# Kernel optimization log

Hardware: AMD Instinct MI355X
Metric: run time of the kernel (lower is better)

Reference implementation:

```python
import jax, jax.numpy as jnp
import numpy as np

N_NODES = 100000
N_EDGES = 1600000
HIDDEN = 64


def setup_inputs() -> dict:
    key = jax.random.key(0)
    ks = jax.random.split(key, 10)
    s = 0.1
    x = jax.random.normal(ks[0], (N_NODES, 1), dtype=jnp.float32)
    edge_index = jax.random.randint(ks[1], (2, N_EDGES), 0, N_NODES, dtype=jnp.int32)
    edge_weight = jnp.ones((N_EDGES,), dtype=jnp.float32)
    f32 = jnp.float32
    return {
        "x": x,
        "edge_weight": edge_weight,
        "Wz": jax.random.normal(ks[2], (1, HIDDEN), f32) * s,
        "bz": jnp.zeros((HIDDEN,), f32),
        "Lz": jax.random.normal(ks[3], (2 * HIDDEN, HIDDEN), f32) * s,
        "lbz": jnp.zeros((HIDDEN,), f32),
        "Wr": jax.random.normal(ks[4], (1, HIDDEN), f32) * s,
        "br": jnp.zeros((HIDDEN,), f32),
        "Lr": jax.random.normal(ks[5], (2 * HIDDEN, HIDDEN), f32) * s,
        "lbr": jnp.zeros((HIDDEN,), f32),
        "Wh": jax.random.normal(ks[6], (1, HIDDEN), f32) * s,
        "bh": jnp.zeros((HIDDEN,), f32),
        "Lh": jax.random.normal(ks[7], (2 * HIDDEN, HIDDEN), f32) * s,
        "lbh": jnp.zeros((HIDDEN,), f32),
        "Wout": jax.random.normal(ks[8], (HIDDEN, 1), f32) * s,
        "bout": jnp.zeros((1,), f32),
        "edge_index": edge_index,
    }


def reference(x, edge_weight, Wz, bz, Lz, lbz, Wr, br, Lr, lbr,
              Wh, bh, Lh, lbh, Wout, bout, edge_index):
    N = x.shape[0]
    hidden = Wz.shape[1]
    src, dst = edge_index[0], edge_index[1]
    # GCN normalization with added self-loops (PyG gcn_norm)
    loop = jnp.arange(N, dtype=src.dtype)
    src2 = jnp.concatenate([src, loop])
    dst2 = jnp.concatenate([dst, loop])
    ew2 = jnp.concatenate([edge_weight, jnp.ones((N,), x.dtype)])
    deg = jax.ops.segment_sum(ew2, dst2, num_segments=N)  # [N]
    dinv = jnp.where(deg > 0, jax.lax.rsqrt(deg), 0.0)
    norm = dinv[src2] * ew2 * dinv[dst2]  # [E+N]

    def gcn(W, b):
        xw = x @ W  # [N, H]
        agg = jax.ops.segment_sum(xw[src2] * norm[:, None], dst2, num_segments=N)
        return agg + b

    # TGCN cell with H0 = 0 (no hidden state passed)
    H = jnp.zeros((N, hidden), x.dtype)
    Z = jax.nn.sigmoid(jnp.concatenate([gcn(Wz, bz), H], axis=1) @ Lz + lbz)
    R = jax.nn.sigmoid(jnp.concatenate([gcn(Wr, br), H], axis=1) @ Lr + lbr)
    Ht = jnp.tanh(jnp.concatenate([gcn(Wh, bh), H * R], axis=1) @ Lh + lbh)
    Hn = Z * H + (1.0 - Z) * Ht
    h = jax.nn.relu(Hn)
    return h @ Wout + bout
```

## Files before the change

kernel.cpp:

```cpp
#include <hip/hip_runtime.h>
#include <math.h>

#define HIDDEN 64
#define RANGE 16384
#define RSHIFT 14
#define NRANGES 7
#define NP 256
#define CAP 1536
#define G 32
#define SUB (NP / G)
#define PACK_SHIFT 17

__global__ __launch_bounds__(512)
void k_part(const int* __restrict__ dst, const int* __restrict__ src,
            const float* __restrict__ ew, uint2* __restrict__ comp,
            int* __restrict__ counts, int E) {
    __shared__ int cur[8];
    if (threadIdx.x < NRANGES) cur[threadIdx.x] = 0;
    __syncthreads();

    const int b = blockIdx.x;
    long long e0 = (((long long)E * b) / NP) & ~3LL;
    long long e1 = (b == NP - 1) ? (long long)E
                                 : ((((long long)E * (b + 1)) / NP) & ~3LL);
    const int nvec = (int)((e1 - e0) >> 2);
    const int4*   dst4 = (const int4*)(dst + e0);
    const int4*   src4 = (const int4*)(src + e0);
    const float4* ew4  = (const float4*)(ew + e0);

    for (int i = threadIdx.x; i < nvec; i += blockDim.x) {
        int4   d = dst4[i];
        int4   s = src4[i];
        float4 t = ew4[i];
        int   dd[4] = {d.x, d.y, d.z, d.w};
        int   ss[4] = {s.x, s.y, s.z, s.w};
        float tt[4] = {t.x, t.y, t.z, t.w};
        #pragma unroll
        for (int j = 0; j < 4; ++j) {
            unsigned u = (unsigned)dd[j];
            int r = (int)(u >> RSHIFT);
            unsigned l = u & (RANGE - 1);
            int pos = atomicAdd(&cur[r], 1);
            if (pos < CAP)
                comp[((size_t)(r * NP + b)) * CAP + pos] =
                    make_uint2((l << PACK_SHIFT) | (unsigned)ss[j],
                               __float_as_uint(tt[j]));
        }
    }
    for (long long e = e0 + ((long long)nvec << 2) + threadIdx.x; e < e1;
         e += blockDim.x) {
        unsigned u = (unsigned)dst[e];
        int r = (int)(u >> RSHIFT);
        unsigned l = u & (RANGE - 1);
        int pos = atomicAdd(&cur[r], 1);
        if (pos < CAP)
            comp[((size_t)(r * NP + b)) * CAP + pos] =
                make_uint2((l << PACK_SHIFT) | (unsigned)src[e],
                           __float_as_uint(ew[e]));
    }
    __syncthreads();
    if (threadIdx.x < NRANGES)
        counts[threadIdx.x * NP + b] = min(cur[threadIdx.x], CAP);
}

__global__ __launch_bounds__(1024)
void k_deg(const uint2* __restrict__ comp, const int* __restrict__ counts,
           float* __restrict__ partials, int nranges) {
    __shared__ float bins[RANGE];
    float4* b4 = (float4*)bins;
    for (int i = threadIdx.x; i < RANGE / 4; i += blockDim.x)
        b4[i] = make_float4(0.f, 0.f, 0.f, 0.f);
    __syncthreads();

    const int r = blockIdx.x % nranges;
    const int c = blockIdx.x / nranges;
    #pragma unroll
    for (int sub = 0; sub < SUB; ++sub) {
        const int b = c * SUB + sub;
        const uint2* sl = comp + ((size_t)(r * NP + b)) * CAP;
        const int n = counts[r * NP + b];
        for (int i = threadIdx.x; i < n; i += blockDim.x) {
            uint2 e = sl[i];
            atomicAdd(&bins[e.x >> PACK_SHIFT], __uint_as_float(e.y));
        }
    }
    __syncthreads();
    float4* outp = (float4*)(partials + ((size_t)c * nranges + r) * RANGE);
    for (int i = threadIdx.x; i < RANGE / 4; i += blockDim.x) outp[i] = b4[i];
}

__global__ void k_node(const float* __restrict__ x, const float* __restrict__ partials,
                       float* __restrict__ dinv, float* __restrict__ w,
                       int N, int nranges,
                       const float* __restrict__ Wz, const float* __restrict__ bz,
                       const float* __restrict__ Lz, const float* __restrict__ lbz,
                       const float* __restrict__ Wh, const float* __restrict__ bh,
                       const float* __restrict__ Lh, const float* __restrict__ lbh,
                       float* __restrict__ coeff) {
    int i = blockIdx.x * blockDim.x + threadIdx.x;
    if (i < N) {
        int r = i >> RSHIFT, local = i & (RANGE - 1);
        const float* p = partials + (size_t)r * RANGE + local;
        float d = 1.0f;
        #pragma unroll
        for (int c = 0; c < G; ++c) d += p[(size_t)c * nranges * RANGE];
        float di = rsqrtf(d);
        dinv[i] = di;
        w[i] = di * x[i];
    }
    if (blockIdx.x == 0 && threadIdx.x < HIDDEN) {
        int j = threadIdx.x;
        float vz = 0.f, cz = 0.f, vh = 0.f, ch = 0.f;
        for (int k = 0; k < HIDDEN; ++k) {
            float lz = Lz[k * HIDDEN + j];
            float lh = Lh[k * HIDDEN + j];
            vz += Wz[k] * lz;
            cz += bz[k] * lz;
            vh += Wh[k] * lh;
            ch += bh[k] * lh;
        }
        coeff[j]       = vz;
        coeff[64 + j]  = cz + lbz[j];
        coeff[128 + j] = vh;
        coeff[192 + j] = ch + lbh[j];
    }
}

__global__ __launch_bounds__(1024)
void k_agg(const uint2* __restrict__ comp, const int* __restrict__ counts,
           const float* __restrict__ w, float* __restrict__ partials, int nranges) {
    __shared__ float bins[RANGE];
    float4* b4 = (float4*)bins;
    for (int i = threadIdx.x; i < RANGE / 4; i += blockDim.x)
        b4[i] = make_float4(0.f, 0.f, 0.f, 0.f);
    __syncthreads();

    const int r = blockIdx.x % nranges;
    const int c = blockIdx.x / nranges;
    #pragma unroll
    for (int sub = 0; sub < SUB; ++sub) {
        const int b = c * SUB + sub;
        const uint2* sl = comp + ((size_t)(r * NP + b)) * CAP;
        const int n = counts[r * NP + b];
        for (int i = threadIdx.x; i < n; i += blockDim.x) {
            uint2 e = sl[i];
            float v = w[e.x & ((1u << PACK_SHIFT) - 1u)] * __uint_as_float(e.y);
            atomicAdd(&bins[e.x >> PACK_SHIFT], v);
        }
    }
    __syncthreads();
    float4* outp = (float4*)(partials + ((size_t)c * nranges + r) * RANGE);
    for (int i = threadIdx.x; i < RANGE / 4; i += blockDim.x) outp[i] = b4[i];
}

__global__ void k_out(const float* __restrict__ partials, const float* __restrict__ dinv,
                      const float* __restrict__ w, const float* __restrict__ coeff,
                      const float* __restrict__ Wout, const float* __restrict__ bout,
                      float* __restrict__ out, int N, int nranges) {
    __shared__ float c[5 * HIDDEN];
    __shared__ float b0;
    if (threadIdx.x < 4 * HIDDEN) c[threadIdx.x] = coeff[threadIdx.x];
    if (threadIdx.x < HIDDEN) c[4 * HIDDEN + threadIdx.x] = Wout[threadIdx.x];
    if (threadIdx.x == 0) b0 = bout[0];
    __syncthreads();
    int i = blockIdx.x * blockDim.x + threadIdx.x;
    if (i < N) {
        int r = i >> RSHIFT, local = i & (RANGE - 1);
        const float* p = partials + (size_t)r * RANGE + local;
        float g = w[i];
        #pragma unroll
        for (int k = 0; k < G; ++k) g += p[(size_t)k * nranges * RANGE];
        float si = dinv[i] * g;
        float acc = b0;
        #pragma unroll
        for (int j = 0; j < HIDDEN; ++j) {
            float zp = fminf(fmaxf(si * c[j] + c[64 + j], -30.f), 30.f);
            float hp = fminf(fmaxf(si * c[128 + j] + c[192 + j], -15.f), 15.f);
            float a  = __expf(2.0f * hp);
            float t  = (a - 1.0f) / (a + 1.0f);
            float zn = 1.0f / (1.0f + __expf(zp));
            float hn = zn * t;
            hn = hn > 0.0f ? hn : 0.0f;
            acc = fmaf(hn, c[256 + j], acc);
        }
        out[i] = acc;
    }
}

extern "C" void kernel_launch(void* const* d_in, const int* in_sizes, int n_in,
                              void* d_out, int out_size, void* d_ws, size_t ws_size,
                              hipStream_t stream) {
    const float* x    = (const float*)d_in[0];
    const float* ew   = (const float*)d_in[1];
    const float* Wz   = (const float*)d_in[2];
    const float* bz   = (const float*)d_in[3];
    const float* Lz   = (const float*)d_in[4];
    const float* lbz  = (const float*)d_in[5];
    const float* Wh   = (const float*)d_in[10];
    const float* bh   = (const float*)d_in[11];
    const float* Lh   = (const float*)d_in[12];
    const float* lbh  = (const float*)d_in[13];
    const float* Wout = (const float*)d_in[14];
    const float* bout = (const float*)d_in[15];
    const int*   eidx = (const int*)d_in[16];

    const int N = in_sizes[0];
    const int E = in_sizes[1];
    const int* src = eidx;
    const int* dst = eidx + E;

    const int nranges = (N + RANGE - 1) / RANGE;

    float* partials = (float*)d_ws;
    uint2* comp     = (uint2*)(partials + (size_t)G * nranges * RANGE);
    float* dinv     = (float*)(comp + (size_t)NRANGES * NP * CAP);
    float* w        = dinv + N;
    float* coeff    = w + N;
    int*   counts   = (int*)(coeff + 4 * HIDDEN);

    const int TB = 256;
    const int grid_bin = nranges * G;

    k_part<<<NP, 512, 0, stream>>>(dst, src, ew, comp, counts, E);
    k_deg<<<grid_bin, 1024, 0, stream>>>(comp, counts, partials, nranges);
    k_node<<<(N + TB - 1) / TB, TB, 0, stream>>>(x, partials, dinv, w, N, nranges,
                                                 Wz, bz, Lz, lbz, Wh, bh, Lh, lbh, coeff);
    k_agg<<<grid_bin, 1024, 0, stream>>>(comp, counts, w, partials, nranges);
    k_out<<<(N + TB - 1) / TB, TB, 0, stream>>>(partials, dinv, w, coeff, Wout, bout,
                                                (float*)d_out, N, nranges);
}
```

Measured before the change: 155.3 us.

## Use fine-grained dst ranges so degree and aggregation fuse with node and output stages

Partitions edges into many small 512-node destination ranges instead of 7 large ones. Each block now owns one range, so degree accumulation writes dinv and w directly, and aggregation computes the final output in place. This removes the partials buffer, the reduction across 32 partial copies, and two kernel launches. The coefficient precompute moves into the partition kernel. The risks are a dynamic per-bucket capacity that could drop edges on skewed inputs, and a smaller grid (~196 blocks) that may underfill the GPU.

```diff
diff --git a/kernel.cpp b/kernel.cpp
--- a/kernel.cpp
+++ b/kernel.cpp
@@ -2,21 +2,24 @@
 #include <math.h>
 
 #define HIDDEN 64
-#define RANGE 16384
-#define RSHIFT 14
-#define NRANGES 7
+#define RANGE 512
+#define RSHIFT 9
 #define NP 256
-#define CAP 1536
-#define G 32
-#define SUB (NP / G)
+#define NRMAX 256
 #define PACK_SHIFT 17
+
 
 __global__ __launch_bounds__(512)
 void k_part(const int* __restrict__ dst, const int* __restrict__ src,
             const float* __restrict__ ew, uint2* __restrict__ comp,
-            int* __restrict__ counts, int E) {
-    __shared__ int cur[8];
-    if (threadIdx.x < NRANGES) cur[threadIdx.x] = 0;
+            int* __restrict__ counts,
+            const float* __restrict__ Wz, const float* __restrict__ bz,
+            const float* __restrict__ Lz, const float* __restrict__ lbz,
+            const float* __restrict__ Wh, const float* __restrict__ bh,
+            const float* __restrict__ Lh, const float* __restrict__ lbh,
+            float* __restrict__ coeff, int E, int nr, int cap) {
+    __shared__ int cur[NRMAX];
+    for (int i = threadIdx.x; i < nr; i += blockDim.x) cur[i] = 0;
     __syncthreads();
 
     const int b = blockIdx.x;
@@ -41,8 +44,8 @@
             int r = (int)(u >> RSHIFT);
             unsigned l = u & (RANGE - 1);
             int pos = atomicAdd(&cur[r], 1);
-            if (pos < CAP)
-                comp[((size_t)(r * NP + b)) * CAP + pos] =
+            if (pos < cap)
+                comp[((size_t)(r * NP + b)) * cap + pos] =
                     make_uint2((l << PACK_SHIFT) | (unsigned)ss[j],
                                __float_as_uint(tt[j]));
         }
@@ -53,62 +56,16 @@
         int r = (int)(u >> RSHIFT);
         unsigned l = u & (RANGE - 1);
         int pos = atomicAdd(&cur[r], 1);
-        if (pos < CAP)
-            comp[((size_t)(r * NP + b)) * CAP + pos] =
+        if (pos < cap)
+            comp[((size_t)(r * NP + b)) * cap + pos] =
                 make_uint2((l << PACK_SHIFT) | (unsigned)src[e],
                            __float_as_uint(ew[e]));
     }
     __syncthreads();
-    if (threadIdx.x < NRANGES)
-        counts[threadIdx.x * NP + b] = min(cur[threadIdx.x], CAP);
-}
-
-__global__ __launch_bounds__(1024)
-void k_deg(const uint2* __restrict__ comp, const int* __restrict__ counts,
-           float* __restrict__ partials, int nranges) {
-    __shared__ float bins[RANGE];
-    float4* b4 = (float4*)bins;
-    for (int i = threadIdx.x; i < RANGE / 4; i += blockDim.x)
-        b4[i] = make_float4(0.f, 0.f, 0.f, 0.f);
-    __syncthreads();
-
-    const int r = blockIdx.x % nranges;
-    const int c = blockIdx.x / nranges;
-    #pragma unroll
-    for (int sub = 0; sub < SUB; ++sub) {
-        const int b = c * SUB + sub;
-        const uint2* sl = comp + ((size_t)(r * NP + b)) * CAP;
-        const int n = counts[r * NP + b];
-        for (int i = threadIdx.x; i < n; i += blockDim.x) {
-            uint2 e = sl[i];
-            atomicAdd(&bins[e.x >> PACK_SHIFT], __uint_as_float(e.y));
-        }
-    }
-    __syncthreads();
-    float4* outp = (float4*)(partials + ((size_t)c * nranges + r) * RANGE);
-    for (int i = threadIdx.x; i < RANGE / 4; i += blockDim.x) outp[i] = b4[i];
-}
-
-__global__ void k_node(const float* __restrict__ x, const float* __restrict__ partials,
-                       float* __restrict__ dinv, float* __restrict__ w,
-                       int N, int nranges,
-                       const float* __restrict__ Wz, const float* __restrict__ bz,
-                       const float* __restrict__ Lz, const float* __restrict__ lbz,
-                       const float* __restrict__ Wh, const float* __restrict__ bh,
-                       const float* __restrict__ Lh, const float* __restrict__ lbh,
-                       float* __restrict__ coeff) {
-    int i = blockIdx.x * blockDim.x + threadIdx.x;
-    if (i < N) {
-        int r = i >> RSHIFT, local = i & (RANGE - 1);
-        const float* p = partials + (size_t)r * RANGE + local;
-        float d = 1.0f;
-        #pragma unroll
-        for (int c = 0; c < G; ++c) d += p[(size_t)c * nranges * RANGE];
-        float di = rsqrtf(d);
-        dinv[i] = di;
-        w[i] = di * x[i];
-    }
-    if (blockIdx.x == 0 && threadIdx.x < HIDDEN) {
+    for (int rr = threadIdx.x; rr < nr; rr += blockDim.x)
+        counts[rr * NP + b] = min(cur[rr], cap);
+
+    if (b == 0 && threadIdx.x < HIDDEN) {
         int j = threadIdx.x;
         float vz = 0.f, cz = 0.f, vh = 0.f, ch = 0.f;
         for (int k = 0; k < HIDDEN; ++k) {
@@ -126,64 +83,88 @@
     }
 }
 
-__global__ __launch_bounds__(1024)
-void k_agg(const uint2* __restrict__ comp, const int* __restrict__ counts,
-           const float* __restrict__ w, float* __restrict__ partials, int nranges) {
+__global__ __launch_bounds__(512)
+void k_degw(const uint2* __restrict__ comp, const int* __restrict__ counts,
+            const float* __restrict__ x, float* __restrict__ dinv,
+            float* __restrict__ w, int N, int cap) {
     __shared__ float bins[RANGE];
-    float4* b4 = (float4*)bins;
-    for (int i = threadIdx.x; i < RANGE / 4; i += blockDim.x)
-        b4[i] = make_float4(0.f, 0.f, 0.f, 0.f);
-    __syncthreads();
-
-    const int r = blockIdx.x % nranges;
-    const int c = blockIdx.x / nranges;
-    #pragma unroll
-    for (int sub = 0; sub < SUB; ++sub) {
-        const int b = c * SUB + sub;
-        const uint2* sl = comp + ((size_t)(r * NP + b)) * CAP;
-        const int n = counts[r * NP + b];
-        for (int i = threadIdx.x; i < n; i += blockDim.x) {
+    __shared__ int cnt[NP];
+    const int r = blockIdx.x;
+    for (int i = threadIdx.x; i < RANGE; i += blockDim.x) bins[i] = 1.0f;
+    for (int i = threadIdx.x; i < NP; i += blockDim.x) cnt[i] = counts[r * NP + i];
+    __syncthreads();
+
+    const int wave = threadIdx.x >> 6, lane = threadIdx.x & 63;
+    const int nw = blockDim.x >> 6;
+    for (int b = wave; b < NP; b += nw) {
+        const int n = cnt[b];
+        const uint2* sl = comp + (size_t)(r * NP + b) * cap;
+        for (int i = lane; i < n; i += 64) {
+            uint2 e = sl[i];
+            atomicAdd(&bins[e.x >> PACK_SHIFT], __uint_as_float(e.y));
+        }
+    }
+    __syncthreads();
+    const int g0 = r << RSHIFT;
+    for (int i = threadIdx.x; i < RANGE; i += blockDim.x) {
+        int g = g0 + i;
+        if (g < N) {
+            float di = rsqrtf(bins[i]);
+            dinv[g] = di;
+            w[g] = di * x[g];
+        }
+    }
+}
+
+__global__ __launch_bounds__(512)
+void k_aggout(const uint2* __restrict__ comp, const int* __restrict__ counts,
+              const float* __restrict__ w, const float* __restrict__ dinv,
+              const float* __restrict__ coeff, const float* __restrict__ Wout,
+              const float* __restrict__ bout, float* __restrict__ out,
+              int N, int cap) {
+    __shared__ float bins[RANGE];
+    __shared__ int cnt[NP];
+    __shared__ float cc[5 * HIDDEN + 1];
+    const int r = blockIdx.x;
+    for (int i = threadIdx.x; i < RANGE; i += blockDim.x) bins[i] = 0.f;
+    for (int i = threadIdx.x; i < NP; i += blockDim.x) cnt[i] = counts[r * NP + i];
+    if (threadIdx.x < 4 * HIDDEN) cc[threadIdx.x] = coeff[threadIdx.x];
+    else if (threadIdx.x < 5 * HIDDEN) cc[threadIdx.x] = Wout[threadIdx.x - 4 * HIDDEN];
+    if (threadIdx.x == 0) cc[5 * HIDDEN] = bout[0];
+    __syncthreads();
+
+    const int wave = threadIdx.x >> 6, lane = threadIdx.x & 63;
+    const int nw = blockDim.x >> 6;
+    for (int b = wave; b < NP; b += nw) {
+        const int n = cnt[b];
+        const uint2* sl = comp + (size_t)(r * NP + b) * cap;
+        for (int i = lane; i < n; i += 64) {
             uint2 e = sl[i];
             float v = w[e.x & ((1u << PACK_SHIFT) - 1u)] * __uint_as_float(e.y);
             atomicAdd(&bins[e.x >> PACK_SHIFT], v);
         }
     }
     __syncthreads();
-    float4* outp = (float4*)(partials + ((size_t)c * nranges + r) * RANGE);
-    for (int i = threadIdx.x; i < RANGE / 4; i += blockDim.x) outp[i] = b4[i];
-}
-
-__global__ void k_out(const float* __restrict__ partials, const float* __restrict__ dinv,
-                      const float* __restrict__ w, const float* __restrict__ coeff,
-                      const float* __restrict__ Wout, const float* __restrict__ bout,
-                      float* __restrict__ out, int N, int nranges) {
-    __shared__ float c[5 * HIDDEN];
-    __shared__ float b0;
-    if (threadIdx.x < 4 * HIDDEN) c[threadIdx.x] = coeff[threadIdx.x];
-    if (threadIdx.x < HIDDEN) c[4 * HIDDEN + threadIdx.x] = Wout[threadIdx.x];
-    if (threadIdx.x == 0) b0 = bout[0];
-    __syncthreads();
-    int i = blockIdx.x * blockDim.x + threadIdx.x;
-    if (i < N) {
-        int r = i >> RSHIFT, local = i & (RANGE - 1);
-        const float* p = partials + (size_t)r * RANGE + local;
-        float g = w[i];
-        #pragma unroll
-        for (int k = 0; k < G; ++k) g += p[(size_t)k * nranges * RANGE];
-        float si = dinv[i] * g;
-        float acc = b0;
-        #pragma unroll
-        for (int j = 0; j < HIDDEN; ++j) {
-            float zp = fminf(fmaxf(si * c[j] + c[64 + j], -30.f), 30.f);
-            float hp = fminf(fmaxf(si * c[128 + j] + c[192 + j], -15.f), 15.f);
-            float a  = __expf(2.0f * hp);
-            float t  = (a - 1.0f) / (a + 1.0f);
-            float zn = 1.0f / (1.0f + __expf(zp));
-            float hn = zn * t;
-            hn = hn > 0.0f ? hn : 0.0f;
-            acc = fmaf(hn, c[256 + j], acc);
-        }
-        out[i] = acc;
+    const int g0 = r << RSHIFT;
+    const float b0 = cc[5 * HIDDEN];
+    for (int i = threadIdx.x; i < RANGE; i += blockDim.x) {
+        int g = g0 + i;
+        if (g < N) {
+            float si = dinv[g] * (bins[i] + w[g]);
+            float acc = b0;
+            #pragma unroll
+            for (int j = 0; j < HIDDEN; ++j) {
+                float zp = fminf(fmaxf(si * cc[j] + cc[64 + j], -30.f), 30.f);
+                float hp = fminf(fmaxf(si * cc[128 + j] + cc[192 + j], -15.f), 15.f);
+                float a  = __expf(2.0f * hp);
+                float t  = (a - 1.0f) / (a + 1.0f);
+                float zn = 1.0f / (1.0f + __expf(zp));
+                float hn = zn * t;
+                hn = hn > 0.0f ? hn : 0.0f;
+                acc = fmaf(hn, cc[256 + j], acc);
+            }
+            out[g] = acc;
+        }
     }
 }
 
@@ -209,23 +190,19 @@
     const int* src = eidx;
     const int* dst = eidx + E;
 
-    const int nranges = (N + RANGE - 1) / RANGE;
-
-    float* partials = (float*)d_ws;
-    uint2* comp     = (uint2*)(partials + (size_t)G * nranges * RANGE);
-    float* dinv     = (float*)(comp + (size_t)NRANGES * NP * CAP);
-    float* w        = dinv + N;
-    float* coeff    = w + N;
-    int*   counts   = (int*)(coeff + 4 * HIDDEN);
-
-    const int TB = 256;
-    const int grid_bin = nranges * G;
-
-    k_part<<<NP, 512, 0, stream>>>(dst, src, ew, comp, counts, E);
-    k_deg<<<grid_bin, 1024, 0, stream>>>(comp, counts, partials, nranges);
-    k_node<<<(N + TB - 1) / TB, TB, 0, stream>>>(x, partials, dinv, w, N, nranges,
-                                                 Wz, bz, Lz, lbz, Wh, bh, Lh, lbh, coeff);
-    k_agg<<<grid_bin, 1024, 0, stream>>>(comp, counts, w, partials, nranges);
-    k_out<<<(N + TB - 1) / TB, TB, 0, stream>>>(partials, dinv, w, coeff, Wout, bout,
-                                                (float*)d_out, N, nranges);
-}
+    const int nr = (N + RANGE - 1) / RANGE;
+    const int cap = (((E / (nr * NP)) * 3) + 35) & ~3;
+
+    uint2* comp   = (uint2*)d_ws;
+    int*   counts = (int*)(comp + (size_t)nr * NP * cap);
+    float* dinv   = (float*)(counts + (size_t)nr * NP);
+    float* w      = dinv + N;
+    float* coeff  = w + N;
+
+    k_part<<<NP, 512, 0, stream>>>(dst, src, ew, comp, counts,
+                                   Wz, bz, Lz, lbz, Wh, bh, Lh, lbh,
+                                   coeff, E, nr, cap);
+    k_degw<<<nr, 512, 0, stream>>>(comp, counts, x, dinv, w, N, cap);
+    k_aggout<<<nr, 512, 0, stream>>>(comp, counts, w, dinv, coeff, Wout, bout,
+                                     (float*)d_out, N, cap);
+}
```

Result: slower. 164.9 us (+6.1%).
